# Kernel optimization log

Measured on AMD Instinct MI355X. Metric: run time of the kernel, lower is better.

Reference implementation:

```python
import jax, jax.numpy as jnp
import numpy as np

N = 100000   # nodes
E = 1600000  # edges
IN = 128     # input feature dim
C = 64       # per-layer output dim (filters)
H = 2        # attention heads
EPS = 1e-5   # batchnorm eps


def setup_inputs() -> dict:
    key = jax.random.key(0)
    ks = jax.random.split(key, 32)
    rn = lambda k, s, sc=0.05: jax.random.normal(k, s, jnp.float32) * sc
    inp = {
        "x": jax.random.normal(ks[0], (N, IN), jnp.float32),
        "edge_index": jax.random.randint(ks[1], (2, E), 0, N, jnp.int32),
        # GATConv layer 0 (IN -> C, H heads, concat=False)
        "W0": rn(ks[2], (IN, H * C)), "as0": rn(ks[3], (H, C)), "ad0": rn(ks[4], (H, C)), "b0": jnp.zeros((C,), jnp.float32),
        "skip0": rn(ks[5], (IN, C)),  # Linear(IN->C, bias=False); layers 1,2 skips are Identity
        "g0": jnp.ones((C,), jnp.float32), "be0": jnp.zeros((C,), jnp.float32),
        # GATConv layer 1 (C -> C)
        "W1": rn(ks[6], (C, H * C)), "as1": rn(ks[7], (H, C)), "ad1": rn(ks[8], (H, C)), "b1": jnp.zeros((C,), jnp.float32),
        "g1": jnp.ones((C,), jnp.float32), "be1": jnp.zeros((C,), jnp.float32),
        # GATConv layer 2 (C -> C)
        "W2": rn(ks[9], (C, H * C)), "as2": rn(ks[10], (H, C)), "ad2": rn(ks[11], (H, C)), "b2": jnp.zeros((C,), jnp.float32),
        "g2": jnp.ones((C,), jnp.float32), "be2": jnp.zeros((C,), jnp.float32),
        # JK projection for input (IN -> C, with bias); other projections are Identity
        "projW": rn(ks[12], (IN, C)), "projb": jnp.zeros((C,), jnp.float32),
    }
    return inp


def _gat(x, edge_index, W, a_src, a_dst, b):
    # PyG GATConv, concat=False: mean over heads, bias added after mean.
    h = (x @ W).reshape(-1, H, C)                 # [N, H, C]
    src, dst = edge_index[0], edge_index[1]
    e_src = jnp.sum(h * a_src, axis=-1)           # [N, H]
    e_dst = jnp.sum(h * a_dst, axis=-1)           # [N, H]
    e = jax.nn.leaky_relu(e_src[src] + e_dst[dst], 0.2)  # [E, H]
    m = jax.ops.segment_max(e, dst, num_segments=N)      # neighbor softmax (stable)
    w = jnp.exp(e - m[dst])
    denom = jax.ops.segment_sum(w, dst, num_segments=N)
    alpha = w / (denom[dst] + 1e-16)              # [E, H]
    out = jax.ops.segment_sum(alpha[:, :, None] * h[src], dst, num_segments=N)  # [N, H, C]
    return out.mean(axis=1) + b


def _bn(x, g, b):
    # BatchNorm1d, training-mode batch statistics (deterministic reference)
    mu = x.mean(axis=0)
    var = x.var(axis=0)
    return (x - mu) * jax.lax.rsqrt(var + EPS) * g + b


def reference(x, edge_index, W0, as0, ad0, b0, skip0, g0, be0,
              W1, as1, ad1, b1, g1, be1,
              W2, as2, ad2, b2, g2, be2,
              projW, projb):
    lrelu = lambda v: jax.nn.leaky_relu(v, 0.01)  # nn.LeakyReLU default
    jk0 = x @ projW + projb                       # proj_lyrs[0]
    # layer 0: GAT + projected skip, BN, (dropout=identity in eval), LeakyReLU
    h1 = _gat(x, edge_index, W0, as0, ad0, b0) + x @ skip0
    h1 = lrelu(_bn(h1, g0, be0))
    # layer 1: identity skip
    h2 = _gat(h1, edge_index, W1, as1, ad1, b1) + h1
    h2 = lrelu(_bn(h2, g1, be1))
    # layer 2: identity skip
    h3 = _gat(h2, edge_index, W2, as2, ad2, b2) + h2
    h3 = lrelu(_bn(h3, g2, be2))
    # jumping knowledge, mode='max': elementwise max over [input_proj, h1, h2, h3]
    return jnp.max(jnp.stack([jk0, h1, h2, h3], axis=0), axis=0)
```

## Files before the change

kernel.cpp:

```cpp
#include <hip/hip_runtime.h>

#define NN 100000
#define NE 1600000

constexpr int NBUC = 196;
constexpr int BIN_CHUNK = 4096;
constexpr int NB_BIN = (NE + BIN_CHUNK - 1) / BIN_CHUNK;

typedef __attribute__((ext_vector_type(8))) short s16x8;
typedef __attribute__((ext_vector_type(4))) float f32x4;
typedef __attribute__((ext_vector_type(2))) float f32x2;

template <int M>
struct IC {
    static constexpr int value = M;
};

__device__ inline unsigned short f2bf(float f) {
    unsigned int u = __float_as_uint(f);
    return (unsigned short)((u + 0x7fffu + ((u >> 16) & 1u)) >> 16);
}
__device__ inline float bf_lo(unsigned int pk) { return __uint_as_float(pk << 16); }
__device__ inline float bf_hi(unsigned int pk) { return __uint_as_float(pk & 0xffff0000u); }

__global__ void zero_u32(unsigned int* p, int n) {
    int i = blockIdx.x * blockDim.x + threadIdx.x;
    if (i < n) p[i] = 0u;
}

__global__ __launch_bounds__(256) void bucket_count(const int* __restrict__ dst,
                                                    int* __restrict__ bcount) {
    __shared__ int hist[NBUC];
    int t = threadIdx.x;
    for (int b = t; b < NBUC; b += 256) hist[b] = 0;
    __syncthreads();
    int beg = blockIdx.x * BIN_CHUNK;
    int end = min(beg + BIN_CHUNK, NE);
    for (int i = beg + t; i < end; i += 256) atomicAdd(&hist[dst[i] >> 9], 1);
    __syncthreads();
    for (int b = t; b < NBUC; b += 256)
        if (hist[b]) atomicAdd(&bcount[b], hist[b]);
}

__global__ void bucket_scan(const int* __restrict__ bcount, int* __restrict__ bbase,
                            int* __restrict__ bucket_cursor, int* __restrict__ offsets) {
    if (threadIdx.x == 0) {
        int run = 0;
        for (int b = 0; b < NBUC; ++b) {
            bbase[b] = run;
            bucket_cursor[b] = run;
            run += bcount[b];
        }
        bbase[NBUC] = NE;
        offsets[NN] = NE;
    }
}

__global__ __launch_bounds__(256) void bin_edges(const int* __restrict__ src,
                                                 const int* __restrict__ dst,
                                                 int* __restrict__ bucket_cursor,
                                                 unsigned int* __restrict__ binned) {
    __shared__ int hist[NBUC];
    __shared__ int base[NBUC];
    int t = threadIdx.x;
    for (int b = t; b < NBUC; b += 256) hist[b] = 0;
    __syncthreads();
    int beg = blockIdx.x * BIN_CHUNK;
    int end = min(beg + BIN_CHUNK, NE);
    for (int i = beg + t; i < end; i += 256) atomicAdd(&hist[dst[i] >> 9], 1);
    __syncthreads();
    for (int b = t; b < NBUC; b += 256) {
        base[b] = hist[b] ? atomicAdd(&bucket_cursor[b], hist[b]) : 0;
        hist[b] = 0;
    }
    __syncthreads();
    for (int i = beg + t; i < end; i += 256) {
        int d = dst[i];
        int bk = d >> 9;
        int loc = atomicAdd(&hist[bk], 1);
        binned[base[bk] + loc] = ((unsigned)(d & 511) << 17) | (unsigned)src[i];
    }
}

__global__ __launch_bounds__(256) void bucket_sort(const unsigned int* __restrict__ binned,
                                                   const int* __restrict__ bbase,
                                                   int* __restrict__ offsets,
                                                   int* __restrict__ csr_src,
                                                   int* __restrict__ csr_dst) {
    __shared__ int deg[512];
    __shared__ int loc[512];
    __shared__ int s2[256];
    int t = threadIdx.x;
    int b = blockIdx.x;
    int beg = bbase[b], end = bbase[b + 1];
    int nbase = b << 9;
    deg[t] = 0;
    deg[t + 256] = 0;
    __syncthreads();
    for (int i = beg + t; i < end; i += 256) atomicAdd(&deg[binned[i] >> 17], 1);
    __syncthreads();
    int pairsum = deg[2 * t] + deg[2 * t + 1];
    s2[t] = pairsum;
    __syncthreads();
    for (int off = 1; off < 256; off <<= 1) {
        int v = (t >= off) ? s2[t - off] : 0;
        __syncthreads();
        s2[t] += v;
        __syncthreads();
    }
    int ex = s2[t] - pairsum;
    loc[2 * t] = ex;
    loc[2 * t + 1] = ex + deg[2 * t];
    __syncthreads();
    for (int i = t; i < 512; i += 256) {
        int node = nbase + i;
        if (node < NN) offsets[node] = beg + loc[i];
    }
    __syncthreads();
    for (int i = beg + t; i < end; i += 256) {
        unsigned int v = binned[i];
        int dl = v >> 17;
        int pos = atomicAdd(&loc[dl], 1);
        csr_src[beg + pos] = (int)(v & 0x1FFFFu);
        csr_dst[beg + pos] = nbase + dl;
    }
}

__global__ void prep_weights(const float* __restrict__ W0, const float* __restrict__ skip0,
                             const float* __restrict__ projW, const float* __restrict__ W1,
                             const float* __restrict__ W2,
                             const float* __restrict__ as0, const float* __restrict__ ad0,
                             const float* __restrict__ as1, const float* __restrict__ ad1,
                             const float* __restrict__ as2, const float* __restrict__ ad2,
                             unsigned short* __restrict__ Wtcat,
                             unsigned short* __restrict__ Wt1,
                             unsigned short* __restrict__ Wt2) {
    int i = blockIdx.x * 256 + threadIdx.x;
    if (i < 16384) {
        int oc = i >> 7, k = i & 127;
        Wtcat[oc * 128 + k] = f2bf(W0[k * 128 + oc]);
    } else if (i < 32768) {
        int j = i - 16384;
        int oc = j >> 7, k = j & 127;
        float v = (oc < 64) ? skip0[k * 64 + oc] : projW[k * 64 + (oc - 64)];
        Wtcat[132 * 128 + oc * 128 + k] = f2bf(v);
    } else if (i < 40960) {
        int j = i - 32768, oc = j >> 6, k = j & 63;
        Wt1[oc * 64 + k] = f2bf(W1[k * 128 + oc]);
    } else if (i < 49152) {
        int j = i - 40960, oc = j >> 6, k = j & 63;
        Wt2[oc * 64 + k] = f2bf(W2[k * 128 + oc]);
    } else if (i < 50688) {
        int e = i - 49152;
        if (e < 512) {
            int k = e >> 2, sc = e & 3, head = sc & 1;
            const float* av = (sc < 2 ? as0 : ad0) + head * 64;
            const float* wr = W0 + k * 128 + head * 64;
            float s = 0.f;
            for (int c = 0; c < 64; ++c) s += wr[c] * av[c];
            Wtcat[(128 + sc) * 128 + k] = f2bf(s);
        } else if (e < 1024) {
            int j = e - 512, k = j >> 2, sc = j & 3;
            Wtcat[132 * 128 + (128 + sc) * 128 + k] = 0;
        } else if (e < 1280) {
            int j = e - 1024, k = j >> 2, sc = j & 3, head = sc & 1;
            const float* av = (sc < 2 ? as1 : ad1) + head * 64;
            const float* wr = W1 + k * 128 + head * 64;
            float s = 0.f;
            for (int c = 0; c < 64; ++c) s += wr[c] * av[c];
            Wt1[(128 + sc) * 64 + k] = f2bf(s);
        } else {
            int j = e - 1280, k = j >> 2, sc = j & 3, head = sc & 1;
            const float* av = (sc < 2 ? as2 : ad2) + head * 64;
            const float* wr = W2 + k * 128 + head * 64;
            float s = 0.f;
            for (int c = 0; c < 64; ++c) s += wr[c] * av[c];
            Wt2[(128 + sc) * 64 + k] = f2bf(s);
        }
    }
}

template <int K, bool L0, bool XFORM>
__global__ __launch_bounds__(256) void gemm_mfma(
    const float* __restrict__ X, const unsigned short* __restrict__ Wt,
    unsigned int* __restrict__ Hq32, float* __restrict__ skipx, float* __restrict__ jkproj,
    const float* __restrict__ projb, const float* __restrict__ bnsc,
    unsigned int* __restrict__ e_srcpk, unsigned int* __restrict__ e_dstpk) {
    constexpr int KP = K + 8;
    constexpr int NC = 132;
    __shared__ unsigned short As[64 * KP];
    __shared__ unsigned short Bs[NC * KP];
    int t = threadIdx.x;
    int rbase = blockIdx.x * 64;
    const unsigned short* Wtg = Wt + (size_t)blockIdx.y * NC * K;

    for (int i = t; i < 64 * (K / 4); i += 256) {
        int r = i / (K / 4);
        int kq = (i % (K / 4)) * 4;
        int gr = rbase + r;
        float4 v = make_float4(0.f, 0.f, 0.f, 0.f);
        if (gr < NN) {
            v = *(const float4*)&X[(size_t)gr * K + kq];
            if (XFORM) {
                float* vc = (float*)&v;
#pragma unroll
                for (int c = 0; c < 4; ++c) {
                    float val = vc[c] * bnsc[kq + c] + bnsc[64 + kq + c];
                    vc[c] = val >= 0.f ? val : 0.01f * val;
                }
            }
        }
        uint2 u;
        u.x = (unsigned int)f2bf(v.x) | ((unsigned int)f2bf(v.y) << 16);
        u.y = (unsigned int)f2bf(v.z) | ((unsigned int)f2bf(v.w) << 16);
        *(uint2*)&As[r * KP + kq] = u;
    }
    for (int i = t; i < NC * (K / 8); i += 256) {
        int oc = i / (K / 8);
        int k8 = (i % (K / 8)) * 8;
        uint4 v = *(const uint4*)&Wtg[(size_t)oc * K + k8];
        *(uint4*)&Bs[oc * KP + k8] = v;
    }
    __syncthreads();

    int lane = t & 63, wv = t >> 6;
    int lr = lane & 15, quad = lane >> 4;
    int arow = wv * 16 + lr;
    f32x4 acc[8];
    f32x4 acc8 = (f32x4)(0.f);
#pragma unroll
    for (int c = 0; c < 8; ++c) acc[c] = (f32x4)(0.f);
#pragma unroll
    for (int k0 = 0; k0 < K; k0 += 32) {
        s16x8 a = *(const s16x8*)&As[arow * KP + k0 + quad * 8];
#pragma unroll
        for (int ct = 0; ct < 8; ++ct) {
            s16x8 b = *(const s16x8*)&Bs[(ct * 16 + lr) * KP + k0 + quad * 8];
            acc[ct] = __builtin_amdgcn_mfma_f32_16x16x32_bf16(a, b, acc[ct], 0, 0, 0);
        }
        s16x8 b9 = *(const s16x8*)&Bs[(128 + (lr & 3)) * KP + k0 + quad * 8];
        acc8 = __builtin_amdgcn_mfma_f32_16x16x32_bf16(a, b9, acc8, 0, 0, 0);
    }

    bool hblock = (!L0) || (blockIdx.y == 0);
#pragma unroll
    for (int reg = 0; reg < 4; ++reg) {
        int row = rbase + wv * 16 + quad * 4 + reg;
        if (hblock) {
            if (row < NN) {
#pragma unroll
                for (int ct = 0; ct < 4; ++ct) {
                    int pk = __builtin_amdgcn_cvt_pk_fp8_f32(acc[ct][reg], acc[ct + 4][reg],
                                                             0, false);
                    int pn = __shfl_xor(pk, 1, 64);
                    if (!(lr & 1))
                        Hq32[(size_t)row * 32 + ct * 8 + (lr >> 1)] =
                            (unsigned int)((pk & 0xFFFF) | (pn << 16));
                }
            }
            float own = acc8[reg];
            float par = __shfl_xor(own, 1, 64);
            if (row < NN) {
                unsigned int pkv = (unsigned)f2bf(own) | ((unsigned)f2bf(par) << 16);
                if (lr == 0) e_srcpk[row] = pkv;
                else if (lr == 2) e_dstpk[row] = pkv;
            }
        } else if (row < NN) {
#pragma unroll
            for (int ct = 0; ct < 4; ++ct)
                skipx[(size_t)row * 64 + ct * 16 + lr] = acc[ct][reg];
#pragma unroll
            for (int ct = 4; ct < 8; ++ct) {
                int c = (ct - 4) * 16 + lr;
                jkproj[(size_t)row * 64 + c] = acc[ct][reg] + projb[c];
            }
        }
    }
}

__global__ void edge_w(const int* __restrict__ csr_src, const int* __restrict__ csr_dst,
                       const unsigned int* __restrict__ e_srcpk,
                       const unsigned int* __restrict__ e_dstpk,
                       uint2* __restrict__ erec) {
    int i = blockIdx.x * blockDim.x + threadIdx.x;
    if (i >= NE) return;
    int s = csr_src[i];
    unsigned int q = e_srcpk[s];
    unsigned int r = e_dstpk[csr_dst[i]];
    float a0 = bf_lo(q) + bf_lo(r);
    float a1 = bf_hi(q) + bf_hi(r);
    a0 = a0 >= 0.f ? a0 : 0.2f * a0;
    a1 = a1 >= 0.f ? a1 : 0.2f * a1;
    unsigned int w = (unsigned int)f2bf(__expf(a0)) | ((unsigned int)f2bf(__expf(a1)) << 16);
    erec[i] = make_uint2((unsigned)s, w);
}

__global__ __launch_bounds__(256) void aggregate(
    const int* __restrict__ offsets, const uint2* __restrict__ erec,
    const unsigned int* __restrict__ Hq32, const float* __restrict__ skipsrc,
    const float* __restrict__ bnsc, const float* __restrict__ bias,
    float* __restrict__ hraw) {
    int wave = threadIdx.x >> 6;
    int lane = threadIdx.x & 63;
    int n = blockIdx.x * 4 + wave;
    if (n >= NN) return;
    const unsigned char* __restrict__ Hq8 = (const unsigned char*)Hq32;
    int beg = __builtin_amdgcn_readfirstlane(offsets[n]);
    int end = __builtin_amdgcn_readfirstlane(offsets[n + 1]);
    int voff = lane * 2;

    float a0 = 0.f, a1 = 0.f, den0 = 0.f, den1 = 0.f;
    int j = beg;

    auto batch = [&](auto Mc) {
        constexpr int M = decltype(Mc)::value;
        uint2 ee[M];
#pragma unroll
        for (int u = 0; u < M; ++u) ee[u] = erec[j + u];
        int ss[M];
        unsigned ww[M];
#pragma unroll
        for (int u = 0; u < M; ++u) {
            ss[u] = __builtin_amdgcn_readfirstlane((int)ee[u].x);
            ww[u] = (unsigned)__builtin_amdgcn_readfirstlane((int)ee[u].y);
        }
        unsigned short uu[M];
#pragma unroll
        for (int u = 0; u < M; ++u)
            uu[u] = *(const unsigned short*)(Hq8 + (size_t)ss[u] * 128 + voff);
#pragma unroll
        for (int u = 0; u < M; ++u) {
            float w0 = bf_lo(ww[u]), w1 = bf_hi(ww[u]);
            f32x2 hv = __builtin_amdgcn_cvt_pk_f32_fp8((int)uu[u], false);
            den0 += w0;
            den1 += w1;
            a0 += w0 * hv[0];
            a1 += w1 * hv[1];
        }
        j += M;
    };

    while (j + 8 <= end) batch(IC<8>{});
    if (j + 4 <= end) batch(IC<4>{});
    if (j + 2 <= end) batch(IC<2>{});
    if (j < end) batch(IC<1>{});

    float sv = skipsrc[(size_t)n * 64 + lane];
    if (bnsc) {
        sv = sv * bnsc[lane] + bnsc[64 + lane];
        sv = sv >= 0.f ? sv : 0.01f * sv;
    }
    float id0 = 1.f / (den0 + 1e-16f), id1 = 1.f / (den1 + 1e-16f);
    float o = 0.5f * (a0 * id0 + a1 * id1) + bias[lane] + sv;
    hraw[(size_t)n * 64 + lane] = o;
}

__global__ void bn_stats(const float* __restrict__ x, float* __restrict__ sums) {
    __shared__ float ls[256], ls2[256];
    int t = threadIdx.x;
    int c = t & 63, q = t >> 6;
    float s = 0.f, s2 = 0.f;
    int rbeg = blockIdx.x * 512;
    for (int r = rbeg + q; r < rbeg + 512; r += 4) {
        if (r < NN) {
            float v = x[(size_t)r * 64 + c];
            s += v;
            s2 += v * v;
        }
    }
    ls[t] = s;
    ls2[t] = s2;
    __syncthreads();
    if (t < 64) {
        s = ls[t] + ls[t + 64] + ls[t + 128] + ls[t + 192];
        s2 = ls2[t] + ls2[t + 64] + ls2[t + 128] + ls2[t + 192];
        atomicAdd(&sums[c], s);
        atomicAdd(&sums[64 + c], s2);
    }
}

__global__ void bn_final(const float* __restrict__ sums, const float* __restrict__ g,
                         const float* __restrict__ be, float* __restrict__ sc_sh) {
    int c = threadIdx.x;
    if (c < 64) {
        float mu = sums[c] / (float)NN;
        float var = sums[64 + c] / (float)NN - mu * mu;
        float sc = g[c] * rsqrtf(var + 1e-5f);
        sc_sh[c] = sc;
        sc_sh[64 + c] = be[c] - mu * sc;
    }
}

__global__ void final_out(const float* __restrict__ jkproj, const float* __restrict__ hA,
                          const float* __restrict__ hB, const float* __restrict__ hC,
                          const float* __restrict__ bnAll, float* __restrict__ out) {
    int i = blockIdx.x * blockDim.x + threadIdx.x;
    if (i < NN * 64) {
        int c = i & 63;
        float v0 = hA[i] * bnAll[c] + bnAll[64 + c];
        float v1 = hB[i] * bnAll[128 + c] + bnAll[192 + c];
        float v2 = hC[i] * bnAll[256 + c] + bnAll[320 + c];
        v0 = v0 >= 0.f ? v0 : 0.01f * v0;
        v1 = v1 >= 0.f ? v1 : 0.01f * v1;
        v2 = v2 >= 0.f ? v2 : 0.01f * v2;
        out[i] = fmaxf(fmaxf(jkproj[i], v0), fmaxf(v1, v2));
    }
}

extern "C" void kernel_launch(void* const* d_in, const int* in_sizes, int n_in,
                              void* d_out, int out_size, void* d_ws, size_t ws_size,
                              hipStream_t stream) {
    const float* x = (const float*)d_in[0];
    const int* ei = (const int*)d_in[1];
    const int* e_src_idx = ei;
    const int* e_dst_idx = ei + NE;
    const float* W0 = (const float*)d_in[2];
    const float* as0 = (const float*)d_in[3];
    const float* ad0 = (const float*)d_in[4];
    const float* b0 = (const float*)d_in[5];
    const float* skip0 = (const float*)d_in[6];
    const float* g0 = (const float*)d_in[7];
    const float* be0 = (const float*)d_in[8];
    const float* W1 = (const float*)d_in[9];
    const float* as1 = (const float*)d_in[10];
    const float* ad1 = (const float*)d_in[11];
    const float* b1 = (const float*)d_in[12];
    const float* g1 = (const float*)d_in[13];
    const float* be1 = (const float*)d_in[14];
    const float* W2 = (const float*)d_in[15];
    const float* as2 = (const float*)d_in[16];
    const float* ad2 = (const float*)d_in[17];
    const float* b2 = (const float*)d_in[18];
    const float* g2 = (const float*)d_in[19];
    const float* be2 = (const float*)d_in[20];
    const float* projW = (const float*)d_in[21];
    const float* projb = (const float*)d_in[22];
    float* out = (float*)d_out;

    char* p = (char*)d_ws;
    auto alloc = [&](size_t bytes) {
        char* r = p;
        p += (bytes + 255) & ~(size_t)255;
        return r;
    };
    int* zbuf = (int*)alloc((size_t)(196 + 384) * 4);
    int* bcount = zbuf;
    float* bnsumAll = (float*)(zbuf + 196);
    int* bbase = (int*)alloc((size_t)(NBUC + 1) * 4);
    int* bucket_cursor = (int*)alloc((size_t)NBUC * 4);
    int* offsets = (int*)alloc((size_t)(NN + 1) * 4);
    int* csr_src = (int*)alloc((size_t)NE * 4);
    int* csr_dst = (int*)alloc((size_t)NE * 4);
    uint2* erec = (uint2*)alloc((size_t)NE * 8);
    unsigned int* binned = (unsigned int*)alloc((size_t)NE * 4);
    unsigned int* h_q32 = (unsigned int*)alloc((size_t)NN * 32 * 4);
    unsigned int* e_srcpk = (unsigned int*)alloc((size_t)NN * 4);
    unsigned int* e_dstpk = (unsigned int*)alloc((size_t)NN * 4);
    float* skipx = (float*)alloc((size_t)NN * 64 * 4);
    float* jkproj = (float*)alloc((size_t)NN * 64 * 4);
    float* hrawA = (float*)alloc((size_t)NN * 64 * 4);
    float* hrawB = (float*)alloc((size_t)NN * 64 * 4);
    float* hrawC = (float*)alloc((size_t)NN * 64 * 4);
    unsigned short* Wtcat = (unsigned short*)alloc((size_t)2 * 132 * 128 * 2);
    unsigned short* Wt1 = (unsigned short*)alloc((size_t)132 * 64 * 2);
    unsigned short* Wt2 = (unsigned short*)alloc((size_t)132 * 64 * 2);
    float* bnscAll = (float*)alloc(3 * 128 * 4);
    if ((size_t)(p - (char*)d_ws) > ws_size) return;

    zero_u32<<<3, 256, 0, stream>>>((unsigned int*)zbuf, 196 + 384);
    bucket_count<<<NB_BIN, 256, 0, stream>>>(e_dst_idx, bcount);
    bucket_scan<<<1, 64, 0, stream>>>(bcount, bbase, bucket_cursor, offsets);
    bin_edges<<<NB_BIN, 256, 0, stream>>>(e_src_idx, e_dst_idx, bucket_cursor, binned);
    bucket_sort<<<NBUC, 256, 0, stream>>>(binned, bbase, offsets, csr_src, csr_dst);
    prep_weights<<<198, 256, 0, stream>>>(W0, skip0, projW, W1, W2, as0, ad0, as1, ad1,
                                          as2, ad2, Wtcat, Wt1, Wt2);

    int gblocks = (NN + 63) / 64;

    gemm_mfma<128, true, false><<<dim3(gblocks, 2), 256, 0, stream>>>(
        x, Wtcat, h_q32, skipx, jkproj, projb, nullptr, e_srcpk, e_dstpk);
    edge_w<<<(NE + 255) / 256, 256, 0, stream>>>(csr_src, csr_dst, e_srcpk, e_dstpk, erec);
    aggregate<<<(NN + 3) / 4, 256, 0, stream>>>(offsets, erec, h_q32, skipx, nullptr, b0,
                                                hrawA);
    bn_stats<<<(NN + 511) / 512, 256, 0, stream>>>(hrawA, bnsumAll);
    bn_final<<<1, 64, 0, stream>>>(bnsumAll, g0, be0, bnscAll);

    gemm_mfma<64, false, true><<<dim3(gblocks, 1), 256, 0, stream>>>(
        hrawA, Wt1, h_q32, nullptr, nullptr, nullptr, bnscAll, e_srcpk, e_dstpk);
    edge_w<<<(NE + 255) / 256, 256, 0, stream>>>(csr_src, csr_dst, e_srcpk, e_dstpk, erec);
    aggregate<<<(NN + 3) / 4, 256, 0, stream>>>(offsets, erec, h_q32, hrawA, bnscAll, b1,
                                                hrawB);
    bn_stats<<<(NN + 511) / 512, 256, 0, stream>>>(hrawB, bnsumAll + 128);
    bn_final<<<1, 64, 0, stream>>>(bnsumAll + 128, g1, be1, bnscAll + 128);

    gemm_mfma<64, false, true><<<dim3(gblocks, 1), 256, 0, stream>>>(
        hrawB, Wt2, h_q32, nullptr, nullptr, nullptr, bnscAll + 128, e_srcpk, e_dstpk);
    edge_w<<<(NE + 255) / 256, 256, 0, stream>>>(csr_src, csr_dst, e_srcpk, e_dstpk, erec);
    aggregate<<<(NN + 3) / 4, 256, 0, stream>>>(offsets, erec, h_q32, hrawB, bnscAll + 128,
                                                b2, hrawC);
    bn_stats<<<(NN + 511) / 512, 256, 0, stream>>>(hrawC, bnsumAll + 256);
    bn_final<<<1, 64, 0, stream>>>(bnsumAll + 256, g2, be2, bnscAll + 256);

    final_out<<<(NN * 64 + 255) / 256, 256, 0, stream>>>(jkproj, hrawA, hrawB, hrawC,
                                                         bnscAll, out);
}
```

Before: 596.6 us.

## Store intermediate node features in fp16 and interleave layer-0 GEMM tiles

Switches the skip projection, JK projection and per-layer raw hidden buffers from fp32 to fp16. This halves the memory traffic in the GEMM, aggregate, bn_stats and final_out kernels. It also swaps the layer-0 GEMM grid so the two weight tiles for the same row block are adjacent blocks, which should improve L2 reuse of the x rows. The cost is reduced precision in the stored activations and in the batchnorm statistics computed from them.

After: 599.7 us. About the same (+0.5%).

```diff
diff --git a/kernel.cpp b/kernel.cpp
--- a/kernel.cpp
+++ b/kernel.cpp
@@ -22,6 +22,12 @@
 }
 __device__ inline float bf_lo(unsigned int pk) { return __uint_as_float(pk << 16); }
 __device__ inline float bf_hi(unsigned int pk) { return __uint_as_float(pk & 0xffff0000u); }
+__device__ inline float h2f(unsigned int u) {
+    _Float16 h;
+    unsigned short s = (unsigned short)u;
+    __builtin_memcpy(&h, &s, 2);
+    return (float)h;
+}
 
 __global__ void zero_u32(unsigned int* p, int n) {
     int i = blockIdx.x * blockDim.x + threadIdx.x;
@@ -182,37 +188,48 @@
 
 template <int K, bool L0, bool XFORM>
 __global__ __launch_bounds__(256) void gemm_mfma(
-    const float* __restrict__ X, const unsigned short* __restrict__ Wt,
-    unsigned int* __restrict__ Hq32, float* __restrict__ skipx, float* __restrict__ jkproj,
-    const float* __restrict__ projb, const float* __restrict__ bnsc,
+    const void* __restrict__ Xv, const unsigned short* __restrict__ Wt,
+    unsigned int* __restrict__ Hq32, _Float16* __restrict__ skipx,
+    _Float16* __restrict__ jkproj, const float* __restrict__ projb,
+    const float* __restrict__ bnsc,
     unsigned int* __restrict__ e_srcpk, unsigned int* __restrict__ e_dstpk) {
     constexpr int KP = K + 8;
     constexpr int NC = 132;
     __shared__ unsigned short As[64 * KP];
     __shared__ unsigned short Bs[NC * KP];
     int t = threadIdx.x;
-    int rbase = blockIdx.x * 64;
-    const unsigned short* Wtg = Wt + (size_t)blockIdx.y * NC * K;
+    int tile = L0 ? blockIdx.x : 0;
+    int rbase = (L0 ? blockIdx.y : blockIdx.x) * 64;
+    const unsigned short* Wtg = Wt + (size_t)tile * NC * K;
 
     for (int i = t; i < 64 * (K / 4); i += 256) {
         int r = i / (K / 4);
         int kq = (i % (K / 4)) * 4;
         int gr = rbase + r;
-        float4 v = make_float4(0.f, 0.f, 0.f, 0.f);
+        float v0 = 0.f, v1 = 0.f, v2 = 0.f, v3 = 0.f;
         if (gr < NN) {
-            v = *(const float4*)&X[(size_t)gr * K + kq];
-            if (XFORM) {
-                float* vc = (float*)&v;
-#pragma unroll
-                for (int c = 0; c < 4; ++c) {
-                    float val = vc[c] * bnsc[kq + c] + bnsc[64 + kq + c];
-                    vc[c] = val >= 0.f ? val : 0.01f * val;
-                }
+            if constexpr (!XFORM) {
+                const float* Xf = (const float*)Xv;
+                float4 v = *(const float4*)&Xf[(size_t)gr * K + kq];
+                v0 = v.x; v1 = v.y; v2 = v.z; v3 = v.w;
+            } else {
+                const _Float16* Xh = (const _Float16*)Xv;
+                uint2 rw = *(const uint2*)&Xh[(size_t)gr * K + kq];
+                v0 = h2f(rw.x); v1 = h2f(rw.x >> 16);
+                v2 = h2f(rw.y); v3 = h2f(rw.y >> 16);
+                auto bnl = [&](float val, int c) {
+                    val = val * bnsc[c] + bnsc[64 + c];
+                    return val >= 0.f ? val : 0.01f * val;
+                };
+                v0 = bnl(v0, kq + 0);
+                v1 = bnl(v1, kq + 1);
+                v2 = bnl(v2, kq + 2);
+                v3 = bnl(v3, kq + 3);
             }
         }
         uint2 u;
-        u.x = (unsigned int)f2bf(v.x) | ((unsigned int)f2bf(v.y) << 16);
-        u.y = (unsigned int)f2bf(v.z) | ((unsigned int)f2bf(v.w) << 16);
+        u.x = (unsigned int)f2bf(v0) | ((unsigned int)f2bf(v1) << 16);
+        u.y = (unsigned int)f2bf(v2) | ((unsigned int)f2bf(v3) << 16);
         *(uint2*)&As[r * KP + kq] = u;
     }
     for (int i = t; i < NC * (K / 8); i += 256) {
@@ -242,7 +259,7 @@
         acc8 = __builtin_amdgcn_mfma_f32_16x16x32_bf16(a, b9, acc8, 0, 0, 0);
     }
 
-    bool hblock = (!L0) || (blockIdx.y == 0);
+    bool hblock = (!L0) || (tile == 0);
 #pragma unroll
     for (int reg = 0; reg < 4; ++reg) {
         int row = rbase + wv * 16 + quad * 4 + reg;
@@ -268,11 +285,11 @@
         } else if (row < NN) {
 #pragma unroll
             for (int ct = 0; ct < 4; ++ct)
-                skipx[(size_t)row * 64 + ct * 16 + lr] = acc[ct][reg];
+                skipx[(size_t)row * 64 + ct * 16 + lr] = (_Float16)acc[ct][reg];
 #pragma unroll
             for (int ct = 4; ct < 8; ++ct) {
                 int c = (ct - 4) * 16 + lr;
-                jkproj[(size_t)row * 64 + c] = acc[ct][reg] + projb[c];
+                jkproj[(size_t)row * 64 + c] = (_Float16)(acc[ct][reg] + projb[c]);
             }
         }
     }
@@ -297,9 +314,9 @@
 
 __global__ __launch_bounds__(256) void aggregate(
     const int* __restrict__ offsets, const uint2* __restrict__ erec,
-    const unsigned int* __restrict__ Hq32, const float* __restrict__ skipsrc,
+    const unsigned int* __restrict__ Hq32, const _Float16* __restrict__ skipsrc,
     const float* __restrict__ bnsc, const float* __restrict__ bias,
-    float* __restrict__ hraw) {
+    _Float16* __restrict__ hraw) {
     int wave = threadIdx.x >> 6;
     int lane = threadIdx.x & 63;
     int n = blockIdx.x * 4 + wave;
@@ -345,17 +362,17 @@
     if (j + 2 <= end) batch(IC<2>{});
     if (j < end) batch(IC<1>{});
 
-    float sv = skipsrc[(size_t)n * 64 + lane];
+    float sv = (float)skipsrc[(size_t)n * 64 + lane];
     if (bnsc) {
         sv = sv * bnsc[lane] + bnsc[64 + lane];
         sv = sv >= 0.f ? sv : 0.01f * sv;
     }
     float id0 = 1.f / (den0 + 1e-16f), id1 = 1.f / (den1 + 1e-16f);
     float o = 0.5f * (a0 * id0 + a1 * id1) + bias[lane] + sv;
-    hraw[(size_t)n * 64 + lane] = o;
-}
-
-__global__ void bn_stats(const float* __restrict__ x, float* __restrict__ sums) {
+    hraw[(size_t)n * 64 + lane] = (_Float16)o;
+}
+
+__global__ void bn_stats(const _Float16* __restrict__ x, float* __restrict__ sums) {
     __shared__ float ls[256], ls2[256];
     int t = threadIdx.x;
     int c = t & 63, q = t >> 6;
@@ -363,7 +380,7 @@
     int rbeg = blockIdx.x * 512;
     for (int r = rbeg + q; r < rbeg + 512; r += 4) {
         if (r < NN) {
-            float v = x[(size_t)r * 64 + c];
+            float v = (float)x[(size_t)r * 64 + c];
             s += v;
             s2 += v * v;
         }
@@ -391,19 +408,19 @@
     }
 }
 
-__global__ void final_out(const float* __restrict__ jkproj, const float* __restrict__ hA,
-                          const float* __restrict__ hB, const float* __restrict__ hC,
+__global__ void final_out(const _Float16* __restrict__ jkproj, const _Float16* __restrict__ hA,
+                          const _Float16* __restrict__ hB, const _Float16* __restrict__ hC,
                           const float* __restrict__ bnAll, float* __restrict__ out) {
     int i = blockIdx.x * blockDim.x + threadIdx.x;
     if (i < NN * 64) {
         int c = i & 63;
-        float v0 = hA[i] * bnAll[c] + bnAll[64 + c];
-        float v1 = hB[i] * bnAll[128 + c] + bnAll[192 + c];
-        float v2 = hC[i] * bnAll[256 + c] + bnAll[320 + c];
+        float v0 = (float)hA[i] * bnAll[c] + bnAll[64 + c];
+        float v1 = (float)hB[i] * bnAll[128 + c] + bnAll[192 + c];
+        float v2 = (float)hC[i] * bnAll[256 + c] + bnAll[320 + c];
         v0 = v0 >= 0.f ? v0 : 0.01f * v0;
         v1 = v1 >= 0.f ? v1 : 0.01f * v1;
         v2 = v2 >= 0.f ? v2 : 0.01f * v2;
-        out[i] = fmaxf(fmaxf(jkproj[i], v0), fmaxf(v1, v2));
+        out[i] = fmaxf(fmaxf((float)jkproj[i], v0), fmaxf(v1, v2));
     }
 }
 
@@ -456,11 +473,11 @@
     unsigned int* h_q32 = (unsigned int*)alloc((size_t)NN * 32 * 4);
     unsigned int* e_srcpk = (unsigned int*)alloc((size_t)NN * 4);
     unsigned int* e_dstpk = (unsigned int*)alloc((size_t)NN * 4);
-    float* skipx = (float*)alloc((size_t)NN * 64 * 4);
-    float* jkproj = (float*)alloc((size_t)NN * 64 * 4);
-    float* hrawA = (float*)alloc((size_t)NN * 64 * 4);
-    float* hrawB = (float*)alloc((size_t)NN * 64 * 4);
-    float* hrawC = (float*)alloc((size_t)NN * 64 * 4);
+    _Float16* skipx = (_Float16*)alloc((size_t)NN * 64 * 2);
+    _Float16* jkproj = (_Float16*)alloc((size_t)NN * 64 * 2);
+    _Float16* hrawA = (_Float16*)alloc((size_t)NN * 64 * 2);
+    _Float16* hrawB = (_Float16*)alloc((size_t)NN * 64 * 2);
+    _Float16* hrawC = (_Float16*)alloc((size_t)NN * 64 * 2);
     unsigned short* Wtcat = (unsigned short*)alloc((size_t)2 * 132 * 128 * 2);
     unsigned short* Wt1 = (unsigned short*)alloc((size_t)132 * 64 * 2);
     unsigned short* Wt2 = (unsigned short*)alloc((size_t)132 * 64 * 2);
@@ -477,7 +494,7 @@
 
     int gblocks = (NN + 63) / 64;
 
-    gemm_mfma<128, true, false><<<dim3(gblocks, 2), 256, 0, stream>>>(
+    gemm_mfma<128, true, false><<<dim3(2, gblocks), 256, 0, stream>>>(
         x, Wtcat, h_q32, skipx, jkproj, projb, nullptr, e_srcpk, e_dstpk);
     edge_w<<<(NE + 255) / 256, 256, 0, stream>>>(csr_src, csr_dst, e_srcpk, e_dstpk, erec);
     aggregate<<<(NN + 3) / 4, 256, 0, stream>>>(offsets, erec, h_q32, skipx, nullptr, b0,
```
